# Optimization experiments

Measured on AMD Instinct MI355X. Metric: run time of the kernel, lower is better.

## Reference

```python
import jax, jax.numpy as jnp
import numpy as np

VOCAB = 32000
DEPTH = 18
INNER = VOCAB - 1
EPS = 1e-9


def setup_inputs() -> dict:
    key = jax.random.key(0)
    k_att, k_w, k_idx, k_sign = jax.random.split(key, 4)
    B, T, D = 4, 16, 512
    att = jax.random.normal(k_att, (B, T, D), dtype=jnp.float32)
    # nn.Linear weight, scaled like kaiming-uniform-ish
    W = jax.random.normal(k_w, (INNER, D), dtype=jnp.float32) * (1.0 / np.sqrt(D))
    n = VOCAB * DEPTH
    path_index = jax.random.randint(k_idx, (n,), 0, INNER, dtype=jnp.int32)
    # Huffman path signs: +1 (left child) or -1 (right child)
    path_sign = jnp.where(jax.random.uniform(k_sign, (n,)) < 0.5, 1.0, -1.0).astype(jnp.float32)
    # bias so that prob = sigmoid(h) for left, 1 - sigmoid(h) for right
    path_bias = (1.0 - path_sign) * 0.5
    return {"att": att, "W": W, "path_index": path_index,
            "path_sign": path_sign, "path_bias": path_bias}


def reference(att, W, path_index, path_sign, path_bias):
    B, T, _ = att.shape
    # Linear (no bias) + sigmoid: [B, T, INNER]
    h = jax.nn.sigmoid(jnp.einsum('btd,nd->btn', att, W))
    # gather along inner-node axis to per-(vocab, depth) path probs
    g = jnp.take(h, path_index, axis=-1) * path_sign + path_bias  # [B, T, VOCAB*DEPTH]
    H = g.reshape(B, T, VOCAB, DEPTH)
    H = jnp.clip(H, EPS, 1.0 - EPS)
    logp = jnp.sum(jnp.log(H), axis=-1)  # [B, T, VOCAB]
    return logp
```

## Files before the change

kernel.cpp:

```cpp
#include <hip/hip_runtime.h>
#include <hip/hip_bf16.h>

#define INNER 31999
#define VOCAB 32000
#define DEPTH 18
#define M_DIM 64
#define K_DIM 512

typedef __attribute__((ext_vector_type(8))) short bf16x8;
typedef __attribute__((ext_vector_type(4))) float f32x4;

__device__ __forceinline__ short f2bf(float f) {
    union { float f; unsigned int u; } c; c.f = f;
    unsigned int u = c.u;
    u += 0x7fffu + ((u >> 16) & 1u);
    return (short)(u >> 16);
}

__device__ __forceinline__ bf16x8 cvt8(float4 lo, float4 hi) {
    bf16x8 r;
    r[0] = f2bf(lo.x); r[1] = f2bf(lo.y); r[2] = f2bf(lo.z); r[3] = f2bf(lo.w);
    r[4] = f2bf(hi.x); r[5] = f2bf(hi.y); r[6] = f2bf(hi.z); r[7] = f2bf(hi.w);
    return r;
}

__global__ __launch_bounds__(256) void conv_att_kernel(
    const float* __restrict__ att, unsigned short* __restrict__ attb)
{
    const int i = (blockIdx.x * 256 + threadIdx.x) * 4;
    const float4 v = *(const float4*)(att + i);
    ushort4 o;
    o.x = (unsigned short)f2bf(v.x);
    o.y = (unsigned short)f2bf(v.y);
    o.z = (unsigned short)f2bf(v.z);
    o.w = (unsigned short)f2bf(v.w);
    *(ushort4*)(attb + i) = o;
}

__global__ __launch_bounds__(128) void gemm_xt_kernel(
    const float* __restrict__ W,
    const unsigned short* __restrict__ attb,
    _Float16* __restrict__ xT)
{
    const int wave = threadIdx.x >> 6;
    const int lane = threadIdx.x & 63;
    const int mrow = lane & 15;
    const int quad = lane >> 4;
    const int n_base = blockIdx.x * 32 + wave * 16;

    const int n = n_base + mrow;
    const int nc = n < INNER ? n : (INNER - 1);
    const float* wp = W + (size_t)nc * K_DIM;

    f32x4 acc[4];
    #pragma unroll
    for (int j = 0; j < 4; j++) acc[j] = (f32x4){0.f, 0.f, 0.f, 0.f};

    #pragma unroll 4
    for (int k0 = 0; k0 < K_DIM; k0 += 32) {
        const int koff = k0 + quad * 8;
        const float4* p = (const float4*)(wp + koff);
        const bf16x8 a = cvt8(p[0], p[1]);
        #pragma unroll
        for (int j = 0; j < 4; j++) {
            const bf16x8 b = *(const bf16x8*)(attb + (j * 16 + mrow) * K_DIM + koff);
            acc[j] = __builtin_amdgcn_mfma_f32_16x16x32_bf16(a, b, acc[j], 0, 0, 0);
        }
    }

    #pragma unroll
    for (int j = 0; j < 4; j++) {
        const int m = j * 16 + mrow;
        #pragma unroll
        for (int r = 0; r < 4; r++)
            xT[(size_t)(n_base + quad * 4 + r) * M_DIM + m] = (_Float16)acc[j][r];
    }
}

__global__ __launch_bounds__(256) void hsoftmax_kernel(
    const _Float16* __restrict__ xT,
    const int*   __restrict__ path_index,
    const float* __restrict__ path_sign,
    float* __restrict__ out)
{
    __shared__ unsigned int packed[32 * DEPTH];
    __shared__ float res[32][M_DIM + 1];

    const int tid = threadIdx.x;
    const int wave = tid >> 6;
    const int lane = tid & 63;
    const int v_base = blockIdx.x * 32;
    const int base = v_base * DEPTH;

    for (int t = tid; t < 32 * DEPTH; t += 256) {
        const unsigned int idx = (unsigned int)path_index[base + t];
        const float s = path_sign[base + t];
        packed[t] = idx | (s < 0.f ? 0x80000000u : 0u);
    }
    __syncthreads();

    for (int i = 0; i < 8; i++) {
        const int vloc = wave * 8 + i;
        float accmin = 0.f;
        float prod = 1.f;
        #pragma unroll
        for (int d = 0; d < DEPTH; d++) {
            const unsigned int p = packed[vloc * DEPTH + d];
            const float x = (float)xT[(p & 0x7fffu) * M_DIM + lane];
            const unsigned int xb = __float_as_uint(x);
            const float negabs = __uint_as_float(xb | 0x80000000u);
            const float y = __uint_as_float(xb ^ (p & 0x80000000u));
            prod *= 1.f + __expf(negabs);
            accmin += fminf(y, 0.f);
        }
        const float r = accmin - __logf(prod);
        res[vloc][lane] = fmaxf(r, -373.1f);
    }
    __syncthreads();

    #pragma unroll
    for (int it = 0; it < 8; it++) {
        const int m = it * 8 + (tid >> 5);
        const int vloc = tid & 31;
        out[(size_t)m * VOCAB + v_base + vloc] = res[vloc][m];
    }
}

extern "C" void kernel_launch(void* const* d_in, const int* in_sizes, int n_in,
                              void* d_out, int out_size, void* d_ws, size_t ws_size,
                              hipStream_t stream) {
    const float* att        = (const float*)d_in[0];
    const float* W          = (const float*)d_in[1];
    const int*   path_index = (const int*)d_in[2];
    const float* path_sign  = (const float*)d_in[3];

    _Float16* xT = (_Float16*)d_ws;
    unsigned short* attb = (unsigned short*)((char*)d_ws + (size_t)VOCAB * M_DIM * 2);
    float* out = (float*)d_out;

    conv_att_kernel<<<32, 256, 0, stream>>>(att, attb);
    gemm_xt_kernel<<<1000, 128, 0, stream>>>(W, attb, xT);
    hsoftmax_kernel<<<1000, 256, 0, stream>>>(xT, path_index, path_sign, out);
}
```

Baseline: 137.6 us.

## Fuse att bf16 conversion into GEMM, use nontemporal W loads, vectorize path gather

Drops the separate att-to-bf16 conversion kernel and converts fp32 att on the fly inside the GEMM, removing one launch and a workspace round trip. W is now read with nontemporal loads and the k-loop unroll is lowered to 2. In the hierarchical softmax kernel each lane gathers two fp16 values with a single 32-bit load, so each wave handles two vocab entries at once with half the gather instructions. The cost is that every GEMM block re-reads fp32 att and converts it again, which doubles that operand's traffic and adds ALU work.

```diff
diff --git a/kernel.cpp b/kernel.cpp
--- a/kernel.cpp
+++ b/kernel.cpp
@@ -9,6 +9,7 @@
 
 typedef __attribute__((ext_vector_type(8))) short bf16x8;
 typedef __attribute__((ext_vector_type(4))) float f32x4;
+typedef __attribute__((ext_vector_type(2))) _Float16 f16x2;
 
 __device__ __forceinline__ short f2bf(float f) {
     union { float f; unsigned int u; } c; c.f = f;
@@ -17,29 +18,16 @@
     return (short)(u >> 16);
 }
 
-__device__ __forceinline__ bf16x8 cvt8(float4 lo, float4 hi) {
+__device__ __forceinline__ bf16x8 cvt8(f32x4 lo, f32x4 hi) {
     bf16x8 r;
-    r[0] = f2bf(lo.x); r[1] = f2bf(lo.y); r[2] = f2bf(lo.z); r[3] = f2bf(lo.w);
-    r[4] = f2bf(hi.x); r[5] = f2bf(hi.y); r[6] = f2bf(hi.z); r[7] = f2bf(hi.w);
+    r[0] = f2bf(lo[0]); r[1] = f2bf(lo[1]); r[2] = f2bf(lo[2]); r[3] = f2bf(lo[3]);
+    r[4] = f2bf(hi[0]); r[5] = f2bf(hi[1]); r[6] = f2bf(hi[2]); r[7] = f2bf(hi[3]);
     return r;
-}
-
-__global__ __launch_bounds__(256) void conv_att_kernel(
-    const float* __restrict__ att, unsigned short* __restrict__ attb)
-{
-    const int i = (blockIdx.x * 256 + threadIdx.x) * 4;
-    const float4 v = *(const float4*)(att + i);
-    ushort4 o;
-    o.x = (unsigned short)f2bf(v.x);
-    o.y = (unsigned short)f2bf(v.y);
-    o.z = (unsigned short)f2bf(v.z);
-    o.w = (unsigned short)f2bf(v.w);
-    *(ushort4*)(attb + i) = o;
 }
 
 __global__ __launch_bounds__(128) void gemm_xt_kernel(
     const float* __restrict__ W,
-    const unsigned short* __restrict__ attb,
+    const float* __restrict__ att,
     _Float16* __restrict__ xT)
 {
     const int wave = threadIdx.x >> 6;
@@ -56,14 +44,17 @@
     #pragma unroll
     for (int j = 0; j < 4; j++) acc[j] = (f32x4){0.f, 0.f, 0.f, 0.f};
 
-    #pragma unroll 4
+    #pragma unroll 2
     for (int k0 = 0; k0 < K_DIM; k0 += 32) {
         const int koff = k0 + quad * 8;
-        const float4* p = (const float4*)(wp + koff);
-        const bf16x8 a = cvt8(p[0], p[1]);
+        const f32x4* p = (const f32x4*)(wp + koff);
+        const f32x4 w0 = __builtin_nontemporal_load(p);
+        const f32x4 w1 = __builtin_nontemporal_load(p + 1);
+        const bf16x8 a = cvt8(w0, w1);
         #pragma unroll
         for (int j = 0; j < 4; j++) {
-            const bf16x8 b = *(const bf16x8*)(attb + (j * 16 + mrow) * K_DIM + koff);
+            const f32x4* bp = (const f32x4*)(att + (j * 16 + mrow) * K_DIM + koff);
+            const bf16x8 b = cvt8(bp[0], bp[1]);
             acc[j] = __builtin_amdgcn_mfma_f32_16x16x32_bf16(a, b, acc[j], 0, 0, 0);
         }
     }
@@ -84,11 +75,13 @@
     float* __restrict__ out)
 {
     __shared__ unsigned int packed[32 * DEPTH];
-    __shared__ float res[32][M_DIM + 1];
+    __shared__ float2 res2[32][33];
 
     const int tid = threadIdx.x;
     const int wave = tid >> 6;
     const int lane = tid & 63;
+    const int half = lane >> 5;
+    const int sub  = lane & 31;
     const int v_base = blockIdx.x * 32;
     const int base = v_base * DEPTH;
 
@@ -99,22 +92,31 @@
     }
     __syncthreads();
 
-    for (int i = 0; i < 8; i++) {
-        const int vloc = wave * 8 + i;
-        float accmin = 0.f;
-        float prod = 1.f;
+    for (int i = 0; i < 4; i++) {
+        const int vloc = wave * 8 + 2 * i + half;
+        float accmin0 = 0.f, accmin1 = 0.f;
+        float prod0 = 1.f, prod1 = 1.f;
         #pragma unroll
         for (int d = 0; d < DEPTH; d++) {
             const unsigned int p = packed[vloc * DEPTH + d];
-            const float x = (float)xT[(p & 0x7fffu) * M_DIM + lane];
-            const unsigned int xb = __float_as_uint(x);
-            const float negabs = __uint_as_float(xb | 0x80000000u);
-            const float y = __uint_as_float(xb ^ (p & 0x80000000u));
-            prod *= 1.f + __expf(negabs);
-            accmin += fminf(y, 0.f);
+            const unsigned int xx = *(const unsigned int*)(
+                (const unsigned short*)xT + (p & 0x7fffu) * M_DIM + sub * 2);
+            union { unsigned int u; f16x2 h; } cv; cv.u = xx;
+            const float x0 = (float)cv.h[0];
+            const float x1 = (float)cv.h[1];
+            const unsigned int sgn = p & 0x80000000u;
+            const unsigned int xb0 = __float_as_uint(x0);
+            const unsigned int xb1 = __float_as_uint(x1);
+            const float e0 = __expf(__uint_as_float(xb0 | 0x80000000u));
+            const float e1 = __expf(__uint_as_float(xb1 | 0x80000000u));
+            prod0 = fmaf(prod0, e0, prod0);
+            prod1 = fmaf(prod1, e1, prod1);
+            accmin0 += fminf(__uint_as_float(xb0 ^ sgn), 0.f);
+            accmin1 += fminf(__uint_as_float(xb1 ^ sgn), 0.f);
         }
-        const float r = accmin - __logf(prod);
-        res[vloc][lane] = fmaxf(r, -373.1f);
+        const float r0 = fmaxf(accmin0 - __logf(prod0), -373.1f);
+        const float r1 = fmaxf(accmin1 - __logf(prod1), -373.1f);
+        res2[vloc][sub] = make_float2(r0, r1);
     }
     __syncthreads();
 
@@ -122,7 +124,7 @@
     for (int it = 0; it < 8; it++) {
         const int m = it * 8 + (tid >> 5);
         const int vloc = tid & 31;
-        out[(size_t)m * VOCAB + v_base + vloc] = res[vloc][m];
+        out[(size_t)m * VOCAB + v_base + vloc] = ((const float*)&res2[vloc][0])[m];
     }
 }
 
@@ -135,10 +137,8 @@
     const float* path_sign  = (const float*)d_in[3];
 
     _Float16* xT = (_Float16*)d_ws;
-    unsigned short* attb = (unsigned short*)((char*)d_ws + (size_t)VOCAB * M_DIM * 2);
     float* out = (float*)d_out;
 
-    conv_att_kernel<<<32, 256, 0, stream>>>(att, attb);
-    gemm_xt_kernel<<<1000, 128, 0, stream>>>(W, attb, xT);
+    gemm_xt_kernel<<<1000, 128, 0, stream>>>(W, att, xT);
     hsoftmax_kernel<<<1000, 256, 0, stream>>>(xT, path_index, path_sign, out);
 }
```

After: 152.3 us. 1.11x slower.
